# Kernel optimization log

Hardware: AMD Instinct MI355X
Metric: run time of the kernel (lower is better)

The kernel has to match this reference:

```python
import jax, jax.numpy as jnp
import numpy as np

HIDDEN = 128
N_NODES = 100000
N_EDGES = 200000
NEG_SLOPE = 0.01  # torch LeakyReLU default


def setup_inputs() -> dict:
    key = jax.random.key(0)
    ks = jax.random.split(key, 12)
    h = HIDDEN
    lim = 1.0 / np.sqrt(h)
    lim3 = 1.0 / np.sqrt(3 * h)
    u = lambda k, shape, l: jax.random.uniform(k, shape, jnp.float32, -l, l)
    return {
        "x_src": jax.random.normal(ks[0], (N_NODES, h), jnp.float32),
        "x_dst": jax.random.normal(ks[1], (N_NODES, h), jnp.float32),
        "edge_index": jax.random.randint(ks[2], (2, N_EDGES), 0, N_NODES, jnp.int64),
        # parent_encoder Linear(h, h)
        "Wp": u(ks[3], (h, h), lim), "bp": u(ks[4], (h,), lim),
        # child_encoder Linear(h, h)
        "Wc": u(ks[5], (h, h), lim), "bc": u(ks[6], (h,), lim),
        # edge_weight_mlp: Linear(3h, h) -> ReLU -> Linear(h, h)
        "W1": u(ks[7], (h, 3 * h), lim3), "b1": u(ks[8], (h,), lim3),
        "W2": u(ks[9], (h, h), lim), "b2": u(ks[10], (h,), lim),
    }


def reference(x_src, x_dst, edge_index, Wp, bp, Wc, bc, W1, b1, W2, b2):
    # gather node feats per edge  [E, h]
    par = x_src[edge_index[0]]
    cld = x_dst[edge_index[1]]
    # dual encoders: Linear + LeakyReLU (Dropout is identity in eval)
    enc_p = jax.nn.leaky_relu(par @ Wp.T + bp, NEG_SLOPE)
    enc_c = jax.nn.leaky_relu(cld @ Wc.T + bc, NEG_SLOPE)
    diff = jnp.abs(par - cld)
    ef = jnp.concatenate([enc_p, enc_c, diff], axis=-1)  # [E, 3h]
    # edge_weight_mlp
    edge_attr = jax.nn.relu(ef @ W1.T + b1) @ W2.T + b2  # [E, h]
    return edge_attr
```

## Files before the change

kernel.cpp:

```cpp
#include <hip/hip_runtime.h>

typedef unsigned short u16;
typedef __attribute__((ext_vector_type(8))) short v8s;
typedef __attribute__((ext_vector_type(4))) float v4f;
typedef __attribute__((ext_vector_type(4))) float f4;

#define HID 128
#define TM  64
#define EFS 392
#define FOS 132

__device__ __forceinline__ u16 f2b(float f) {
    union { float f; unsigned u; } v; v.f = f;
    unsigned u = v.u;
    u += 0x7fffu + ((u >> 16) & 1u);
    return (u16)(u >> 16);
}

#define MFMA(A, B, C) __builtin_amdgcn_mfma_f32_16x16x32_bf16(A, B, C, 0, 0, 0)

__global__ void cvt_weights(const float* __restrict__ Wp, const float* __restrict__ Wc,
                            const float* __restrict__ W1, const float* __restrict__ W2,
                            u16* __restrict__ dst)
{
    int i = blockIdx.x * 256 + threadIdx.x;
    const float* s; int off;
    if (i < 4096)       { s = Wp; off = 0; }
    else if (i < 8192)  { s = Wc; off = 4096; }
    else if (i < 20480) { s = W1; off = 8192; }
    else                { s = W2; off = 20480; }
    int j = i - off;
    f4 v = ((const f4*)s)[j];
    u16* d = dst + (size_t)i * 4;
    d[0] = f2b(v[0]); d[1] = f2b(v[1]); d[2] = f2b(v[2]); d[3] = f2b(v[3]);
}

__global__ __launch_bounds__(512, 6) void edge_attr_kernel(
    const float* __restrict__ x_src, const float* __restrict__ x_dst,
    const int* __restrict__ ei,
    const u16* __restrict__ wsW,
    const float* __restrict__ bp, const float* __restrict__ bc,
    const float* __restrict__ b1, const float* __restrict__ b2,
    float* __restrict__ out, int E)
{
    __shared__ __align__(16) u16 sEF[TM * EFS];

    const u16* wsWp = wsW;
    const u16* wsWc = wsW + 16384;
    const u16* wsW1 = wsW + 32768;
    const u16* wsW2 = wsW + 81920;

    const int t  = threadIdx.x;
    const int e0 = blockIdx.x * TM;
    const int* ei0 = ei;
    const int* ei1 = ei + E;

    #pragma unroll
    for (int i = 0; i < 2; ++i) {
        int idx = t + i * 512;
        int r = idx >> 4;
        int c = (idx & 15) << 3;
        int e = e0 + r; if (e >= E) e = E - 1;
        const f4* ps = (const f4*)(x_src + (size_t)ei0[e] * HID + c);
        const f4* qs = (const f4*)(x_dst + (size_t)ei1[e] * HID + c);
        f4 p0 = ps[0], p1 = ps[1];
        f4 q0 = qs[0], q1 = qs[1];
        v8s pb, qb, db;
        #pragma unroll
        for (int j = 0; j < 4; ++j) {
            pb[j]     = (short)f2b(p0[j]);
            pb[j + 4] = (short)f2b(p1[j]);
            qb[j]     = (short)f2b(q0[j]);
            qb[j + 4] = (short)f2b(q1[j]);
            db[j]     = (short)f2b(fabsf(p0[j] - q0[j]));
            db[j + 4] = (short)f2b(fabsf(p1[j] - q1[j]));
        }
        *(v8s*)&sEF[r * EFS       + c] = pb;
        *(v8s*)&sEF[r * EFS + 128 + c] = qb;
        *(v8s*)&sEF[r * EFS + 256 + c] = db;
    }
    __syncthreads();

    const int lane = t & 63;
    const int ln = lane & 15;
    const int lq = lane >> 4;
    const int w  = t >> 6;
    const int r0 = (w >> 2) * 32;
    const int c0 = (w & 3) * 32;

    v4f aP[2][2], aC[2][2];
    float bpv[2], bcv[2];
    #pragma unroll
    for (int nt = 0; nt < 2; ++nt) {
        bpv[nt] = bp[c0 + nt * 16 + ln];
        bcv[nt] = bc[c0 + nt * 16 + ln];
    }
    {
        v8s B[2][4];
        #pragma unroll
        for (int nt = 0; nt < 2; ++nt) {
            int n = c0 + nt * 16 + ln;
            #pragma unroll
            for (int kt = 0; kt < 4; ++kt)
                B[nt][kt] = *(const v8s*)(wsWp + (size_t)n * HID + kt * 32 + lq * 8);
        }
        #pragma unroll
        for (int mt = 0; mt < 2; ++mt) {
            const int rb = (r0 + mt * 16 + ln) * EFS + lq * 8;
            v8s A[4];
            #pragma unroll
            for (int kt = 0; kt < 4; ++kt) A[kt] = *(const v8s*)&sEF[rb + kt * 32];
            #pragma unroll
            for (int nt = 0; nt < 2; ++nt) {
                aP[mt][nt] = (v4f){0.f, 0.f, 0.f, 0.f};
                #pragma unroll
                for (int kt = 0; kt < 4; ++kt) aP[mt][nt] = MFMA(A[kt], B[nt][kt], aP[mt][nt]);
            }
        }
    }
    #pragma unroll
    for (int nt = 0; nt < 2; ++nt) {
        v8s B[4];
        int n = c0 + nt * 16 + ln;
        #pragma unroll
        for (int kt = 0; kt < 4; ++kt)
            B[kt] = *(const v8s*)(wsWc + (size_t)n * HID + kt * 32 + lq * 8);
        #pragma unroll
        for (int mt = 0; mt < 2; ++mt) {
            const int rb = (r0 + mt * 16 + ln) * EFS + 128 + lq * 8;
            v8s A[4];
            #pragma unroll
            for (int kt = 0; kt < 4; ++kt) A[kt] = *(const v8s*)&sEF[rb + kt * 32];
            aC[mt][nt] = (v4f){0.f, 0.f, 0.f, 0.f};
            #pragma unroll
            for (int kt = 0; kt < 4; ++kt) aC[mt][nt] = MFMA(A[kt], B[kt], aC[mt][nt]);
        }
    }
    __syncthreads();
    #pragma unroll
    for (int mt = 0; mt < 2; ++mt)
        #pragma unroll
        for (int nt = 0; nt < 2; ++nt)
            #pragma unroll
            for (int rg = 0; rg < 4; ++rg) {
                int row = r0 + mt * 16 + lq * 4 + rg;
                int col = c0 + nt * 16 + ln;
                float vp = aP[mt][nt][rg] + bpv[nt];
                vp = vp > 0.f ? vp : 0.01f * vp;
                sEF[row * EFS + col] = f2b(vp);
                float vc = aC[mt][nt][rg] + bcv[nt];
                vc = vc > 0.f ? vc : 0.01f * vc;
                sEF[row * EFS + 128 + col] = f2b(vc);
            }
    __syncthreads();

    {
        float b1v[2];
        #pragma unroll
        for (int nt = 0; nt < 2; ++nt) b1v[nt] = b1[c0 + nt * 16 + ln];
        v4f acc[2][2];
        #pragma unroll
        for (int mt = 0; mt < 2; ++mt)
            #pragma unroll
            for (int nt = 0; nt < 2; ++nt) acc[mt][nt] = (v4f){0.f, 0.f, 0.f, 0.f};
        #pragma unroll
        for (int ktc = 0; ktc < 3; ++ktc) {
            v8s B[2][4];
            #pragma unroll
            for (int nt = 0; nt < 2; ++nt) {
                int n = c0 + nt * 16 + ln;
                #pragma unroll
                for (int k4 = 0; k4 < 4; ++k4)
                    B[nt][k4] = *(const v8s*)(wsW1 + (size_t)n * 384 + ktc * 128 + k4 * 32 + lq * 8);
            }
            #pragma unroll
            for (int mt = 0; mt < 2; ++mt) {
                const int rb = (r0 + mt * 16 + ln) * EFS + ktc * 128 + lq * 8;
                v8s A[4];
                #pragma unroll
                for (int k4 = 0; k4 < 4; ++k4) A[k4] = *(const v8s*)&sEF[rb + k4 * 32];
                #pragma unroll
                for (int nt = 0; nt < 2; ++nt)
                    #pragma unroll
                    for (int k4 = 0; k4 < 4; ++k4) acc[mt][nt] = MFMA(A[k4], B[nt][k4], acc[mt][nt]);
            }
        }
        __syncthreads();
        #pragma unroll
        for (int mt = 0; mt < 2; ++mt)
            #pragma unroll
            for (int nt = 0; nt < 2; ++nt)
                #pragma unroll
                for (int rg = 0; rg < 4; ++rg) {
                    int row = r0 + mt * 16 + lq * 4 + rg;
                    int col = c0 + nt * 16 + ln;
                    float v = acc[mt][nt][rg] + b1v[nt];
                    sEF[row * EFS + 256 + col] = f2b(fmaxf(v, 0.f));
                }
        __syncthreads();
    }

    {
        float b2v[2];
        #pragma unroll
        for (int nt = 0; nt < 2; ++nt) b2v[nt] = b2[c0 + nt * 16 + ln];
        v4f acc[2][2];
        v8s B[2][4];
        #pragma unroll
        for (int nt = 0; nt < 2; ++nt) {
            int n = c0 + nt * 16 + ln;
            #pragma unroll
            for (int kt = 0; kt < 4; ++kt)
                B[nt][kt] = *(const v8s*)(wsW2 + (size_t)n * HID + kt * 32 + lq * 8);
        }
        #pragma unroll
        for (int mt = 0; mt < 2; ++mt) {
            const int rb = (r0 + mt * 16 + ln) * EFS + 256 + lq * 8;
            v8s A[4];
            #pragma unroll
            for (int kt = 0; kt < 4; ++kt) A[kt] = *(const v8s*)&sEF[rb + kt * 32];
            #pragma unroll
            for (int nt = 0; nt < 2; ++nt) {
                acc[mt][nt] = (v4f){0.f, 0.f, 0.f, 0.f};
                #pragma unroll
                for (int kt = 0; kt < 4; ++kt) acc[mt][nt] = MFMA(A[kt], B[nt][kt], acc[mt][nt]);
            }
        }
        __syncthreads();
        float* sF = (float*)sEF;
        #pragma unroll
        for (int mt = 0; mt < 2; ++mt)
            #pragma unroll
            for (int nt = 0; nt < 2; ++nt)
                #pragma unroll
                for (int rg = 0; rg < 4; ++rg) {
                    int row = r0 + mt * 16 + lq * 4 + rg;
                    int col = c0 + nt * 16 + ln;
                    sF[row * FOS + col] = acc[mt][nt][rg] + b2v[nt];
                }
        __syncthreads();
    }

    {
        const float* sF = (const float*)sEF;
        #pragma unroll
        for (int i = 0; i < 4; ++i) {
            int idx = t + i * 512;
            int r = idx >> 5;
            int c = (idx & 31) << 2;
            int e = e0 + r;
            if (e < E)
                *(f4*)(out + (size_t)e * HID + c) = *(const f4*)&sF[r * FOS + c];
        }
    }
}

extern "C" void kernel_launch(void* const* d_in, const int* in_sizes, int n_in,
                              void* d_out, int out_size, void* d_ws, size_t ws_size,
                              hipStream_t stream) {
    const float* x_src = (const float*)d_in[0];
    const float* x_dst = (const float*)d_in[1];
    const int*   ei    = (const int*)d_in[2];
    const float* Wp    = (const float*)d_in[3];
    const float* bp    = (const float*)d_in[4];
    const float* Wc    = (const float*)d_in[5];
    const float* bc    = (const float*)d_in[6];
    const float* W1    = (const float*)d_in[7];
    const float* b1    = (const float*)d_in[8];
    const float* W2    = (const float*)d_in[9];
    const float* b2    = (const float*)d_in[10];
    float* out = (float*)d_out;
    u16* wsW = (u16*)d_ws;

    int E = in_sizes[2] / 2;

    cvt_weights<<<96, 256, 0, stream>>>(Wp, Wc, W1, W2, wsW);

    int blocks = (E + TM - 1) / TM;
    edge_attr_kernel<<<blocks, 512, 0, stream>>>(
        x_src, x_dst, ei, wsW, bp, bc, b1, b2, out, E);
}
```

Baseline: 332.8 us.

## Make edge kernel persistent with register-prefetched gathers of next tile

Converts the one-block-per-tile edge kernel into a persistent grid of 512 blocks that loop over tiles. Each iteration issues the index loads and row gathers for the next tile into registers, so they overlap the current tile's MFMA stages. It also swaps __syncthreads for a custom barrier that waits only on LDS counters, and uses nontemporal output stores. The cost is more live registers (launch bounds lowered from 6 to 4) and fewer resident blocks, which may reduce latency hiding.

```diff
diff --git a/kernel.cpp b/kernel.cpp
--- a/kernel.cpp
+++ b/kernel.cpp
@@ -9,6 +9,7 @@
 #define TM  64
 #define EFS 392
 #define FOS 132
+#define PBLK 512
 
 __device__ __forceinline__ u16 f2b(float f) {
     union { float f; unsigned u; } v; v.f = f;
@@ -18,6 +19,12 @@
 }
 
 #define MFMA(A, B, C) __builtin_amdgcn_mfma_f32_16x16x32_bf16(A, B, C, 0, 0, 0)
+
+__device__ __forceinline__ void barw() {
+    asm volatile("s_waitcnt lgkmcnt(0)" ::: "memory");
+    __builtin_amdgcn_s_barrier();
+    asm volatile("" ::: "memory");
+}
 
 __global__ void cvt_weights(const float* __restrict__ Wp, const float* __restrict__ Wc,
                             const float* __restrict__ W1, const float* __restrict__ W2,
@@ -35,13 +42,13 @@
     d[0] = f2b(v[0]); d[1] = f2b(v[1]); d[2] = f2b(v[2]); d[3] = f2b(v[3]);
 }
 
-__global__ __launch_bounds__(512, 6) void edge_attr_kernel(
+__global__ __launch_bounds__(512, 4) void edge_attr_kernel(
     const float* __restrict__ x_src, const float* __restrict__ x_dst,
     const int* __restrict__ ei,
     const u16* __restrict__ wsW,
     const float* __restrict__ bp, const float* __restrict__ bc,
     const float* __restrict__ b1, const float* __restrict__ b2,
-    float* __restrict__ out, int E)
+    float* __restrict__ out, int E, int ntiles)
 {
     __shared__ __align__(16) u16 sEF[TM * EFS];
 
@@ -51,35 +58,11 @@
     const u16* wsW2 = wsW + 81920;
 
     const int t  = threadIdx.x;
-    const int e0 = blockIdx.x * TM;
     const int* ei0 = ei;
     const int* ei1 = ei + E;
 
-    #pragma unroll
-    for (int i = 0; i < 2; ++i) {
-        int idx = t + i * 512;
-        int r = idx >> 4;
-        int c = (idx & 15) << 3;
-        int e = e0 + r; if (e >= E) e = E - 1;
-        const f4* ps = (const f4*)(x_src + (size_t)ei0[e] * HID + c);
-        const f4* qs = (const f4*)(x_dst + (size_t)ei1[e] * HID + c);
-        f4 p0 = ps[0], p1 = ps[1];
-        f4 q0 = qs[0], q1 = qs[1];
-        v8s pb, qb, db;
-        #pragma unroll
-        for (int j = 0; j < 4; ++j) {
-            pb[j]     = (short)f2b(p0[j]);
-            pb[j + 4] = (short)f2b(p1[j]);
-            qb[j]     = (short)f2b(q0[j]);
-            qb[j + 4] = (short)f2b(q1[j]);
-            db[j]     = (short)f2b(fabsf(p0[j] - q0[j]));
-            db[j + 4] = (short)f2b(fabsf(p1[j] - q1[j]));
-        }
-        *(v8s*)&sEF[r * EFS       + c] = pb;
-        *(v8s*)&sEF[r * EFS + 128 + c] = qb;
-        *(v8s*)&sEF[r * EFS + 256 + c] = db;
-    }
-    __syncthreads();
+    const int gr = t >> 4;
+    const int gc = (t & 15) << 3;
 
     const int lane = t & 63;
     const int ln = lane & 15;
@@ -88,104 +71,105 @@
     const int r0 = (w >> 2) * 32;
     const int c0 = (w & 3) * 32;
 
-    v4f aP[2][2], aC[2][2];
-    float bpv[2], bcv[2];
-    #pragma unroll
-    for (int nt = 0; nt < 2; ++nt) {
-        bpv[nt] = bp[c0 + nt * 16 + ln];
-        bcv[nt] = bc[c0 + nt * 16 + ln];
-    }
-    {
-        v8s B[2][4];
+    int iA0, iA1, iB0, iB1;
+    f4 PA0, PA1, QA0, QA1, PB0, PB1, QB0, QB1;
+
+    auto pre_issue = [&](int tile) {
+        int e0 = tile * TM;
+        int ea = e0 + gr;       if (ea >= E) ea = E - 1;
+        int eb = e0 + gr + 32;  if (eb >= E) eb = E - 1;
+        iA0 = ei0[ea]; iA1 = ei1[ea];
+        iB0 = ei0[eb]; iB1 = ei1[eb];
+    };
+    auto issue_rows = [&]() {
+        const f4* pa = (const f4*)(x_src + (size_t)iA0 * HID + gc);
+        const f4* qa = (const f4*)(x_dst + (size_t)iA1 * HID + gc);
+        const f4* pb = (const f4*)(x_src + (size_t)iB0 * HID + gc);
+        const f4* qb = (const f4*)(x_dst + (size_t)iB1 * HID + gc);
+        PA0 = pa[0]; PA1 = pa[1]; QA0 = qa[0]; QA1 = qa[1];
+        PB0 = pb[0]; PB1 = pb[1]; QB0 = qb[0]; QB1 = qb[1];
+    };
+    auto convert_store = [&]() {
+        #pragma unroll
+        for (int i = 0; i < 2; ++i) {
+            int r = gr + i * 32;
+            f4 p0 = i ? PB0 : PA0, p1 = i ? PB1 : PA1;
+            f4 q0 = i ? QB0 : QA0, q1 = i ? QB1 : QA1;
+            v8s pbv, qbv, dbv;
+            #pragma unroll
+            for (int j = 0; j < 4; ++j) {
+                pbv[j]     = (short)f2b(p0[j]);
+                pbv[j + 4] = (short)f2b(p1[j]);
+                qbv[j]     = (short)f2b(q0[j]);
+                qbv[j + 4] = (short)f2b(q1[j]);
+                dbv[j]     = (short)f2b(fabsf(p0[j] - q0[j]));
+                dbv[j + 4] = (short)f2b(fabsf(p1[j] - q1[j]));
+            }
+            *(v8s*)&sEF[r * EFS       + gc] = pbv;
+            *(v8s*)&sEF[r * EFS + 128 + gc] = qbv;
+            *(v8s*)&sEF[r * EFS + 256 + gc] = dbv;
+        }
+    };
+
+    int tile = blockIdx.x;
+    if (tile < ntiles) { pre_issue(tile); issue_rows(); }
+
+    for (; tile < ntiles; tile += PBLK) {
+        int nxt = tile + PBLK;
+        if (nxt < ntiles) pre_issue(nxt);
+        convert_store();
+        barw();
+        if (nxt < ntiles) issue_rows();
+
+        v4f aP[2][2], aC[2][2];
+        float bpv[2], bcv[2];
         #pragma unroll
         for (int nt = 0; nt < 2; ++nt) {
-            int n = c0 + nt * 16 + ln;
-            #pragma unroll
-            for (int kt = 0; kt < 4; ++kt)
-                B[nt][kt] = *(const v8s*)(wsWp + (size_t)n * HID + kt * 32 + lq * 8);
-        }
-        #pragma unroll
-        for (int mt = 0; mt < 2; ++mt) {
-            const int rb = (r0 + mt * 16 + ln) * EFS + lq * 8;
-            v8s A[4];
-            #pragma unroll
-            for (int kt = 0; kt < 4; ++kt) A[kt] = *(const v8s*)&sEF[rb + kt * 32];
-            #pragma unroll
-            for (int nt = 0; nt < 2; ++nt) {
-                aP[mt][nt] = (v4f){0.f, 0.f, 0.f, 0.f};
-                #pragma unroll
-                for (int kt = 0; kt < 4; ++kt) aP[mt][nt] = MFMA(A[kt], B[nt][kt], aP[mt][nt]);
-            }
-        }
-    }
-    #pragma unroll
-    for (int nt = 0; nt < 2; ++nt) {
-        v8s B[4];
-        int n = c0 + nt * 16 + ln;
-        #pragma unroll
-        for (int kt = 0; kt < 4; ++kt)
-            B[kt] = *(const v8s*)(wsWc + (size_t)n * HID + kt * 32 + lq * 8);
-        #pragma unroll
-        for (int mt = 0; mt < 2; ++mt) {
-            const int rb = (r0 + mt * 16 + ln) * EFS + 128 + lq * 8;
-            v8s A[4];
-            #pragma unroll
-            for (int kt = 0; kt < 4; ++kt) A[kt] = *(const v8s*)&sEF[rb + kt * 32];
-            aC[mt][nt] = (v4f){0.f, 0.f, 0.f, 0.f};
-            #pragma unroll
-            for (int kt = 0; kt < 4; ++kt) aC[mt][nt] = MFMA(A[kt], B[kt], aC[mt][nt]);
-        }
-    }
-    __syncthreads();
-    #pragma unroll
-    for (int mt = 0; mt < 2; ++mt)
-        #pragma unroll
-        for (int nt = 0; nt < 2; ++nt)
-            #pragma unroll
-            for (int rg = 0; rg < 4; ++rg) {
-                int row = r0 + mt * 16 + lq * 4 + rg;
-                int col = c0 + nt * 16 + ln;
-                float vp = aP[mt][nt][rg] + bpv[nt];
-                vp = vp > 0.f ? vp : 0.01f * vp;
-                sEF[row * EFS + col] = f2b(vp);
-                float vc = aC[mt][nt][rg] + bcv[nt];
-                vc = vc > 0.f ? vc : 0.01f * vc;
-                sEF[row * EFS + 128 + col] = f2b(vc);
-            }
-    __syncthreads();
-
-    {
-        float b1v[2];
-        #pragma unroll
-        for (int nt = 0; nt < 2; ++nt) b1v[nt] = b1[c0 + nt * 16 + ln];
-        v4f acc[2][2];
-        #pragma unroll
-        for (int mt = 0; mt < 2; ++mt)
-            #pragma unroll
-            for (int nt = 0; nt < 2; ++nt) acc[mt][nt] = (v4f){0.f, 0.f, 0.f, 0.f};
-        #pragma unroll
-        for (int ktc = 0; ktc < 3; ++ktc) {
+            bpv[nt] = bp[c0 + nt * 16 + ln];
+            bcv[nt] = bc[c0 + nt * 16 + ln];
+        }
+        {
             v8s B[2][4];
             #pragma unroll
             for (int nt = 0; nt < 2; ++nt) {
                 int n = c0 + nt * 16 + ln;
                 #pragma unroll
-                for (int k4 = 0; k4 < 4; ++k4)
-                    B[nt][k4] = *(const v8s*)(wsW1 + (size_t)n * 384 + ktc * 128 + k4 * 32 + lq * 8);
+                for (int kt = 0; kt < 4; ++kt)
+                    B[nt][kt] = *(const v8s*)(wsWp + (size_t)n * HID + kt * 32 + lq * 8);
             }
             #pragma unroll
             for (int mt = 0; mt < 2; ++mt) {
-                const int rb = (r0 + mt * 16 + ln) * EFS + ktc * 128 + lq * 8;
+                const int rb = (r0 + mt * 16 + ln) * EFS + lq * 8;
                 v8s A[4];
                 #pragma unroll
-                for (int k4 = 0; k4 < 4; ++k4) A[k4] = *(const v8s*)&sEF[rb + k4 * 32];
-                #pragma unroll
-                for (int nt = 0; nt < 2; ++nt)
-                    #pragma unroll
-                    for (int k4 = 0; k4 < 4; ++k4) acc[mt][nt] = MFMA(A[k4], B[nt][k4], acc[mt][nt]);
-            }
-        }
-        __syncthreads();
+                for (int kt = 0; kt < 4; ++kt) A[kt] = *(const v8s*)&sEF[rb + kt * 32];
+                #pragma unroll
+                for (int nt = 0; nt < 2; ++nt) {
+                    aP[mt][nt] = (v4f){0.f, 0.f, 0.f, 0.f};
+                    #pragma unroll
+                    for (int kt = 0; kt < 4; ++kt) aP[mt][nt] = MFMA(A[kt], B[nt][kt], aP[mt][nt]);
+                }
+            }
+        }
+        #pragma unroll
+        for (int nt = 0; nt < 2; ++nt) {
+            v8s B[4];
+            int n = c0 + nt * 16 + ln;
+            #pragma unroll
+            for (int kt = 0; kt < 4; ++kt)
+                B[kt] = *(const v8s*)(wsWc + (size_t)n * HID + kt * 32 + lq * 8);
+            #pragma unroll
+            for (int mt = 0; mt < 2; ++mt) {
+                const int rb = (r0 + mt * 16 + ln) * EFS + 128 + lq * 8;
+                v8s A[4];
+                #pragma unroll
+                for (int kt = 0; kt < 4; ++kt) A[kt] = *(const v8s*)&sEF[rb + kt * 32];
+                aC[mt][nt] = (v4f){0.f, 0.f, 0.f, 0.f};
+                #pragma unroll
+                for (int kt = 0; kt < 4; ++kt) aC[mt][nt] = MFMA(A[kt], B[kt], aC[mt][nt]);
+            }
+        }
+        barw();
         #pragma unroll
         for (int mt = 0; mt < 2; ++mt)
             #pragma unroll
@@ -194,64 +178,118 @@
                 for (int rg = 0; rg < 4; ++rg) {
                     int row = r0 + mt * 16 + lq * 4 + rg;
                     int col = c0 + nt * 16 + ln;
-                    float v = acc[mt][nt][rg] + b1v[nt];
-                    sEF[row * EFS + 256 + col] = f2b(fmaxf(v, 0.f));
-                }
-        __syncthreads();
-    }
-
-    {
-        float b2v[2];
-        #pragma unroll
-        for (int nt = 0; nt < 2; ++nt) b2v[nt] = b2[c0 + nt * 16 + ln];
-        v4f acc[2][2];
-        v8s B[2][4];
-        #pragma unroll
-        for (int nt = 0; nt < 2; ++nt) {
-            int n = c0 + nt * 16 + ln;
-            #pragma unroll
-            for (int kt = 0; kt < 4; ++kt)
-                B[nt][kt] = *(const v8s*)(wsW2 + (size_t)n * HID + kt * 32 + lq * 8);
-        }
-        #pragma unroll
-        for (int mt = 0; mt < 2; ++mt) {
-            const int rb = (r0 + mt * 16 + ln) * EFS + 256 + lq * 8;
-            v8s A[4];
-            #pragma unroll
-            for (int kt = 0; kt < 4; ++kt) A[kt] = *(const v8s*)&sEF[rb + kt * 32];
+                    float vp = aP[mt][nt][rg] + bpv[nt];
+                    vp = vp > 0.f ? vp : 0.01f * vp;
+                    sEF[row * EFS + col] = f2b(vp);
+                    float vc = aC[mt][nt][rg] + bcv[nt];
+                    vc = vc > 0.f ? vc : 0.01f * vc;
+                    sEF[row * EFS + 128 + col] = f2b(vc);
+                }
+        barw();
+
+        {
+            float b1v[2];
+            #pragma unroll
+            for (int nt = 0; nt < 2; ++nt) b1v[nt] = b1[c0 + nt * 16 + ln];
+            v4f acc[2][2];
+            #pragma unroll
+            for (int mt = 0; mt < 2; ++mt)
+                #pragma unroll
+                for (int nt = 0; nt < 2; ++nt) acc[mt][nt] = (v4f){0.f, 0.f, 0.f, 0.f};
+            #pragma unroll
+            for (int ktc = 0; ktc < 3; ++ktc) {
+                v8s B[2][4];
+                #pragma unroll
+                for (int nt = 0; nt < 2; ++nt) {
+                    int n = c0 + nt * 16 + ln;
+                    #pragma unroll
+                    for (int k4 = 0; k4 < 4; ++k4)
+                        B[nt][k4] = *(const v8s*)(wsW1 + (size_t)n * 384 + ktc * 128 + k4 * 32 + lq * 8);
+                }
+                #pragma unroll
+                for (int mt = 0; mt < 2; ++mt) {
+                    const int rb = (r0 + mt * 16 + ln) * EFS + ktc * 128 + lq * 8;
+                    v8s A[4];
+                    #pragma unroll
+                    for (int k4 = 0; k4 < 4; ++k4) A[k4] = *(const v8s*)&sEF[rb + k4 * 32];
+                    #pragma unroll
+                    for (int nt = 0; nt < 2; ++nt)
+                        #pragma unroll
+                        for (int k4 = 0; k4 < 4; ++k4) acc[mt][nt] = MFMA(A[k4], B[nt][k4], acc[mt][nt]);
+                }
+            }
+            barw();
+            #pragma unroll
+            for (int mt = 0; mt < 2; ++mt)
+                #pragma unroll
+                for (int nt = 0; nt < 2; ++nt)
+                    #pragma unroll
+                    for (int rg = 0; rg < 4; ++rg) {
+                        int row = r0 + mt * 16 + lq * 4 + rg;
+                        int col = c0 + nt * 16 + ln;
+                        float v = acc[mt][nt][rg] + b1v[nt];
+                        sEF[row * EFS + 256 + col] = f2b(fmaxf(v, 0.f));
+                    }
+            barw();
+        }
+
+        {
+            float b2v[2];
+            #pragma unroll
+            for (int nt = 0; nt < 2; ++nt) b2v[nt] = b2[c0 + nt * 16 + ln];
+            v4f acc[2][2];
+            v8s B[2][4];
             #pragma unroll
             for (int nt = 0; nt < 2; ++nt) {
-                acc[mt][nt] = (v4f){0.f, 0.f, 0.f, 0.f};
-                #pragma unroll
-                for (int kt = 0; kt < 4; ++kt) acc[mt][nt] = MFMA(A[kt], B[nt][kt], acc[mt][nt]);
-            }
-        }
-        __syncthreads();
-        float* sF = (float*)sEF;
-        #pragma unroll
-        for (int mt = 0; mt < 2; ++mt)
-            #pragma unroll
-            for (int nt = 0; nt < 2; ++nt)
-                #pragma unroll
-                for (int rg = 0; rg < 4; ++rg) {
-                    int row = r0 + mt * 16 + lq * 4 + rg;
-                    int col = c0 + nt * 16 + ln;
-                    sF[row * FOS + col] = acc[mt][nt][rg] + b2v[nt];
-                }
-        __syncthreads();
-    }
-
-    {
-        const float* sF = (const float*)sEF;
-        #pragma unroll
-        for (int i = 0; i < 4; ++i) {
-            int idx = t + i * 512;
-            int r = idx >> 5;
-            int c = (idx & 31) << 2;
-            int e = e0 + r;
-            if (e < E)
-                *(f4*)(out + (size_t)e * HID + c) = *(const f4*)&sF[r * FOS + c];
-        }
+                int n = c0 + nt * 16 + ln;
+                #pragma unroll
+                for (int kt = 0; kt < 4; ++kt)
+                    B[nt][kt] = *(const v8s*)(wsW2 + (size_t)n * HID + kt * 32 + lq * 8);
+            }
+            #pragma unroll
+            for (int mt = 0; mt < 2; ++mt) {
+                const int rb = (r0 + mt * 16 + ln) * EFS + 256 + lq * 8;
+                v8s A[4];
+                #pragma unroll
+                for (int kt = 0; kt < 4; ++kt) A[kt] = *(const v8s*)&sEF[rb + kt * 32];
+                #pragma unroll
+                for (int nt = 0; nt < 2; ++nt) {
+                    acc[mt][nt] = (v4f){0.f, 0.f, 0.f, 0.f};
+                    #pragma unroll
+                    for (int kt = 0; kt < 4; ++kt) acc[mt][nt] = MFMA(A[kt], B[nt][kt], acc[mt][nt]);
+                }
+            }
+            barw();
+            float* sF = (float*)sEF;
+            #pragma unroll
+            for (int mt = 0; mt < 2; ++mt)
+                #pragma unroll
+                for (int nt = 0; nt < 2; ++nt)
+                    #pragma unroll
+                    for (int rg = 0; rg < 4; ++rg) {
+                        int row = r0 + mt * 16 + lq * 4 + rg;
+                        int col = c0 + nt * 16 + ln;
+                        sF[row * FOS + col] = acc[mt][nt][rg] + b2v[nt];
+                    }
+            barw();
+        }
+
+        {
+            const float* sF = (const float*)sEF;
+            int e0s = tile * TM;
+            #pragma unroll
+            for (int i = 0; i < 4; ++i) {
+                int idx2 = t + i * 512;
+                int r = idx2 >> 5;
+                int c = (idx2 & 31) << 2;
+                int e = e0s + r;
+                if (e < E) {
+                    f4 vv = *(const f4*)&sF[r * FOS + c];
+                    __builtin_nontemporal_store(vv, (f4*)(out + (size_t)e * HID + c));
+                }
+            }
+        }
+        barw();
     }
 }
 
@@ -273,10 +311,11 @@
     u16* wsW = (u16*)d_ws;
 
     int E = in_sizes[2] / 2;
+    int ntiles = (E + TM - 1) / TM;
 
     cvt_weights<<<96, 256, 0, stream>>>(Wp, Wc, W1, W2, wsW);
 
-    int blocks = (E + TM - 1) / TM;
+    int blocks = ntiles < PBLK ? ntiles : PBLK;
     edge_attr_kernel<<<blocks, 512, 0, stream>>>(
-        x_src, x_dst, ei, wsW, bp, bc, b1, b2, out, E);
-}
+        x_src, x_dst, ei, wsW, bp, bc, b1, b2, out, E, ntiles);
+}
```

New measurement: 390.6 us. +17.4%, slower.
